# Optimization experiments

Measured on AMD Instinct MI355X. Metric: run time of the kernel, lower is better.

Reference implementation:

```python
import jax, jax.numpy as jnp
import numpy as np

B, C, W, H = 4, 64, 64, 64
CQK = C // 8  # query/key channels


def setup_inputs() -> dict:
    key = jax.random.key(0)
    ks = jax.random.split(key, 8)
    s = 0.05
    return {
        "x": jax.random.normal(ks[0], (B, C, W, H), jnp.float32),
        "Wq": jax.random.normal(ks[1], (CQK, C), jnp.float32) * s,
        "bq": jax.random.normal(ks[2], (CQK,), jnp.float32) * s,
        "Wk": jax.random.normal(ks[3], (CQK, C), jnp.float32) * s,
        "bk": jax.random.normal(ks[4], (CQK,), jnp.float32) * s,
        "Wv": jax.random.normal(ks[5], (C, C), jnp.float32) * s,
        "bv": jax.random.normal(ks[6], (C,), jnp.float32) * s,
        # torch init is zeros; use a nonzero value so the attention path is exercised
        "gamma": jax.random.normal(ks[7], (1,), jnp.float32) * s,
    }


def reference(x, Wq, bq, Wk, bk, Wv, bv, gamma):
    b, c, w, h = x.shape
    n = w * h
    xf = x.reshape(b, c, n)  # B, C, N
    # 1x1 convs == per-pixel linear maps
    q = jnp.einsum("oc,bcn->bno", Wq, xf) + bq           # B, N, Cqk
    k = jnp.einsum("oc,bcn->bon", Wk, xf) + bk[:, None]   # B, Cqk, N
    energy = jnp.einsum("bno,bom->bnm", q, k)             # B, N, N
    attn = jax.nn.softmax(energy, axis=-1)                # B, N, N
    v = jnp.einsum("oc,bcn->bon", Wv, xf) + bv[:, None]   # B, C, N
    # out[b,c,j] = sum_n v[b,c,n] * attn[j,n]  (bmm with attention^T)
    out = jnp.einsum("bcn,bjn->bcj", v, attn)
    out = out.reshape(b, c, w, h)
    return gamma * out + x
```

## Files before the change

### kernel.cpp

```cpp
#include <hip/hip_runtime.h>

typedef short s16x8 __attribute__((ext_vector_type(8)));
typedef float f32x4 __attribute__((ext_vector_type(4)));
typedef float f32x16 __attribute__((ext_vector_type(16)));
typedef unsigned u32x4 __attribute__((ext_vector_type(4)));

#define BB 4
#define NN 4096
#define LOG2E 1.4426950408889634f

__device__ __forceinline__ unsigned short f2bf(float f) {
    unsigned int u = __builtin_bit_cast(unsigned int, f);
    u += 0x7fff + ((u >> 16) & 1);
    return (unsigned short)(u >> 16);
}

__device__ __forceinline__ unsigned pk2(float lo, float hi) {
    return __builtin_amdgcn_perm(__builtin_bit_cast(unsigned, hi),
                                 __builtin_bit_cast(unsigned, lo), 0x07060302u);
}

__device__ __forceinline__ void pl32swap(unsigned &a, unsigned &b) {
    asm volatile("v_permlane32_swap_b32 %0, %1" : "+v"(a), "+v"(b));
}

__global__ __launch_bounds__(256) void proj_kernel(
    const float* __restrict__ x,
    const float* __restrict__ Wq, const float* __restrict__ bq,
    const float* __restrict__ Wk, const float* __restrict__ bk,
    const float* __restrict__ Wv, const float* __restrict__ bv,
    unsigned short* __restrict__ Qw, unsigned short* __restrict__ Kw,
    unsigned short* __restrict__ Vc)
{
    __shared__ __attribute__((aligned(16))) unsigned short sW[80 * 72];
    __shared__ __attribute__((aligned(16))) unsigned short xT[64 * 72];
    __shared__ float sb[80];

    int tid = threadIdx.x;
    int b  = blockIdx.x >> 6;
    int n0 = (blockIdx.x & 63) << 6;

    for (int i = tid; i < 1280; i += 256) {
        int o = i >> 4, c4 = (i & 15) << 2;
        const float* src = (o < 8) ? &Wq[o * 64 + c4]
                         : ((o < 16) ? &Wk[(o - 8) * 64 + c4]
                                     : &Wv[(o - 16) * 64 + c4]);
        float4 v = *(const float4*)src;
        float sc = (o < 8) ? LOG2E : 1.f;
        sW[o * 72 + c4 + 0] = f2bf(v.x * sc);
        sW[o * 72 + c4 + 1] = f2bf(v.y * sc);
        sW[o * 72 + c4 + 2] = f2bf(v.z * sc);
        sW[o * 72 + c4 + 3] = f2bf(v.w * sc);
    }
    if (tid < 80)
        sb[tid] = (tid < 8) ? bq[tid] * LOG2E
                            : ((tid < 16) ? bk[tid - 8] : bv[tid - 16]);
    for (int i = tid; i < 1024; i += 256) {
        int c = i >> 4, p4 = (i & 15) << 2;
        float4 v = *(const float4*)&x[(((size_t)b * 64 + c) << 12) + n0 + p4];
        xT[(p4 + 0) * 72 + c] = f2bf(v.x);
        xT[(p4 + 1) * 72 + c] = f2bf(v.y);
        xT[(p4 + 2) * 72 + c] = f2bf(v.z);
        xT[(p4 + 3) * 72 + c] = f2bf(v.w);
    }
    __syncthreads();

    int w = tid >> 6, l = tid & 63, g = l >> 4, q16 = l & 15;
    int pix = w * 16 + q16;

    s16x8 bf0 = *(const s16x8*)&xT[pix * 72 + g * 8];
    s16x8 bf1 = *(const s16x8*)&xT[pix * 72 + 32 + g * 8];

    s16x8 a0[5], a1[5];
#pragma unroll
    for (int ot = 0; ot < 5; ++ot) {
        a0[ot] = *(const s16x8*)&sW[(ot * 16 + q16) * 72 + g * 8];
        a1[ot] = *(const s16x8*)&sW[(ot * 16 + q16) * 72 + 32 + g * 8];
    }
    __syncthreads();

    unsigned short* sV = xT;
    size_t base16 = ((size_t)(b << 12) + n0 + pix) << 4;

#pragma unroll
    for (int ot = 0; ot < 5; ++ot) {
        f32x4 acc = {0.f, 0.f, 0.f, 0.f};
        acc = __builtin_amdgcn_mfma_f32_16x16x32_bf16(a0[ot], bf0, acc, 0, 0, 0);
        acc = __builtin_amdgcn_mfma_f32_16x16x32_bf16(a1[ot], bf1, acc, 0, 0, 0);
#pragma unroll
        for (int r = 0; r < 4; ++r) {
            int orow = ot * 16 + g * 4 + r;
            unsigned short hv = f2bf(acc[r] + sb[orow]);
            if (ot == 0) {
                if (orow < 8) {
                    Qw[base16 + orow] = hv;
                    Qw[base16 + orow + 8] = 0;
                } else {
                    Kw[base16 + orow - 8] = hv;
                    Kw[base16 + orow] = 0;
                }
            } else {
                sV[(orow - 16) * 72 + pix] = hv;
            }
        }
    }
    __syncthreads();

#pragma unroll
    for (int i = tid; i < 512; i += 256) {
        int jj = i >> 6, c = i & 63;
        u32x4 v = *(const u32x4*)&sV[c * 72 + jj * 8];
        int jglob = ((blockIdx.x & 63) << 3) + jj;
        *(u32x4*)&Vc[(((size_t)b * 512 + jglob) * 64 + c) * 8] = v;
    }
}

__global__ __launch_bounds__(512, 2) void attn_kernel(
    const unsigned short* __restrict__ Qw, const unsigned short* __restrict__ Kw,
    const unsigned short* __restrict__ Vc, const float* __restrict__ x,
    const float* __restrict__ gamma, float* __restrict__ outp)
{
    __shared__ __attribute__((aligned(16))) float sO[64 * 36];
    __shared__ float sL[8 * 32];
    __shared__ float sGL[32];

    int tid = threadIdx.x;
    int w = tid >> 6, l = tid & 63, r31 = l & 31, hi = l >> 5;
    int p = blockIdx.x;
    int xcd = p & 7, kgrp = p >> 3;
    int b = xcd >> 1;
    int n0 = (((kgrp << 1) | (xcd & 1))) << 5;
    float gm = gamma[0];

    s16x8 qf = *(const s16x8*)((const char*)Qw + ((size_t)b << 17)
                               + ((size_t)(n0 + r31) << 5) + (hi << 4));
    const char* KbW = (const char*)Kw + ((size_t)b << 17) + (w << 14)
                    + (r31 << 5) + (hi << 4);
    const char* VcB = (const char*)Vc + ((size_t)b << 19) + (w << 16)
                    + (hi << 10) + (r31 << 4);

    f32x16 zz;
#pragma unroll
    for (int i = 0; i < 16; ++i) zz[i] = 0.f;

    f32x16 acc0, acc1;
#pragma unroll
    for (int i = 0; i < 16; ++i) { acc0[i] = 0.f; acc1[i] = 0.f; }
    float la = 0.f;

    s16x8 K_a, A0_a, A1_a, B0_a, B1_a;
    s16x8 K_b, A0_b, A1_b, B0_b, B1_b;

#define LOADSET(S, kp, vp) do {                                             \
        K_##S  = *(const s16x8*)(kp);                                       \
        A0_##S = *(const s16x8*)(vp);                                       \
        B0_##S = *(const s16x8*)((vp) + 512);                               \
        A1_##S = *(const s16x8*)((vp) + 2048);                              \
        B1_##S = *(const s16x8*)((vp) + 2560);                              \
    } while (0)

#define STEP(S) do {                                                        \
        f32x16 E = __builtin_amdgcn_mfma_f32_32x32x16_bf16(K_##S, qf, zz, 0, 0, 0); \
        _Pragma("unroll")                                                   \
        for (int i = 0; i < 16; ++i) E[i] = __builtin_amdgcn_exp2f(E[i]);   \
        la += (((E[0] + E[1]) + (E[2] + E[3])) + ((E[4] + E[5]) + (E[6] + E[7]))) \
            + (((E[8] + E[9]) + (E[10] + E[11])) + ((E[12] + E[13]) + (E[14] + E[15]))); \
        unsigned x0 = pk2(E[0], E[1]),   x1 = pk2(E[2], E[3]);              \
        unsigned x2 = pk2(E[4], E[5]),   x3 = pk2(E[6], E[7]);              \
        unsigned x4 = pk2(E[8], E[9]),   x5 = pk2(E[10], E[11]);            \
        unsigned x6 = pk2(E[12], E[13]), x7 = pk2(E[14], E[15]);            \
        pl32swap(x0, x2); pl32swap(x1, x3);                                 \
        pl32swap(x4, x6); pl32swap(x5, x7);                                 \
        u32x4 u0 = {x0, x1, x2, x3}, u1 = {x4, x5, x6, x7};                 \
        s16x8 pf0 = __builtin_bit_cast(s16x8, u0);                          \
        s16x8 pf1 = __builtin_bit_cast(s16x8, u1);                          \
        acc0 = __builtin_amdgcn_mfma_f32_32x32x16_bf16(A0_##S, pf0, acc0, 0, 0, 0); \
        acc0 = __builtin_amdgcn_mfma_f32_32x32x16_bf16(A1_##S, pf1, acc0, 0, 0, 0); \
        acc1 = __builtin_amdgcn_mfma_f32_32x32x16_bf16(B0_##S, pf0, acc1, 0, 0, 0); \
        acc1 = __builtin_amdgcn_mfma_f32_32x32x16_bf16(B1_##S, pf1, acc1, 0, 0, 0); \
    } while (0)

    const char* ka = KbW;
    const char* va = VcB;
    const char* kb = KbW + 1024;
    const char* vb = VcB + 4096;

    LOADSET(a, ka, va);
    LOADSET(b, kb, vb);

#pragma unroll 1
    for (int tt = 0; tt < 7; ++tt) {
        ka += 2048; va += 8192;
        STEP(a);
        LOADSET(a, ka, va);
        kb += 2048; vb += 8192;
        STEP(b);
        LOADSET(b, kb, vb);
    }
    STEP(a);
    STEP(b);

#undef LOADSET
#undef STEP

    la += __shfl_xor(la, 32);
    if (l < 32) sL[w * 32 + l] = la;

#pragma unroll
    for (int s = 0; s < 8; ++s) {
        __syncthreads();
#pragma unroll
        for (int B = 0; B < 8; ++B) {
            if (((w + s) & 7) == B) {
                const int R2 = B & 3;
                float e0 = (B < 4) ? acc0[R2 * 4 + 0] : acc1[R2 * 4 + 0];
                float e1 = (B < 4) ? acc0[R2 * 4 + 1] : acc1[R2 * 4 + 1];
                float e2 = (B < 4) ? acc0[R2 * 4 + 2] : acc1[R2 * 4 + 2];
                float e3 = (B < 4) ? acc0[R2 * 4 + 3] : acc1[R2 * 4 + 3];
                float* pp = &sO[(B * 8 + hi * 4) * 36 + r31];
                if (s == 0) {
                    pp[0] = e0; pp[36] = e1; pp[72] = e2; pp[108] = e3;
                } else {
                    pp[0] += e0; pp[36] += e1; pp[72] += e2; pp[108] += e3;
                }
            }
        }
    }
    __syncthreads();

    if (tid < 32) {
        float L = 0.f;
#pragma unroll
        for (int wk2 = 0; wk2 < 8; ++wk2) L += sL[wk2 * 32 + tid];
        sGL[tid] = gm / L;
    }
    __syncthreads();

    {
        int c = tid >> 3, qc = tid & 7;
        float4 o4 = *(const float4*)&sO[c * 36 + qc * 4];
        float4 g4 = *(const float4*)&sGL[qc * 4];
        size_t idx = (((size_t)b * 64 + c) << 12) + n0 + qc * 4;
        float4 x4v = *(const float4*)&x[idx];
        o4.x = o4.x * g4.x + x4v.x;
        o4.y = o4.y * g4.y + x4v.y;
        o4.z = o4.z * g4.z + x4v.z;
        o4.w = o4.w * g4.w + x4v.w;
        *(float4*)&outp[idx] = o4;
    }
}

extern "C" void kernel_launch(void* const* d_in, const int* in_sizes, int n_in,
                              void* d_out, int out_size, void* d_ws, size_t ws_size,
                              hipStream_t stream) {
    const float* x     = (const float*)d_in[0];
    const float* Wq    = (const float*)d_in[1];
    const float* bq    = (const float*)d_in[2];
    const float* Wk    = (const float*)d_in[3];
    const float* bk    = (const float*)d_in[4];
    const float* Wv    = (const float*)d_in[5];
    const float* bv    = (const float*)d_in[6];
    const float* gamma = (const float*)d_in[7];
    float* out = (float*)d_out;

    unsigned short* Qw = (unsigned short*)d_ws;
    unsigned short* Kw = Qw + (size_t)BB * NN * 16;
    unsigned short* Vc = Kw + (size_t)BB * NN * 16;

    proj_kernel<<<256, 256, 0, stream>>>(x, Wq, bq, Wk, bk, Wv, bv, Qw, Kw, Vc);
    attn_kernel<<<512, 512, 0, stream>>>(Qw, Kw, Vc, x, gamma, out);
}
```

Baseline: 29.74 us.

## Process 64 query rows per block with 16 waves sharing a KV split

Each attention block now handles 64 query rows instead of 32. It uses 1024 threads arranged as 2 query groups by 8 KV-split waves, which halves the grid to 256 blocks. The two query groups read the same K/V ranges, so that traffic can hit in cache, and the per-block fixed costs of reduction and epilogue are amortised over twice the work. In exchange there are fewer blocks for 256 CUs, a heavier block with barrier syncs across 16 waves, and a possibly lower occupancy bound.

```diff
diff --git a/kernel.cpp b/kernel.cpp
--- a/kernel.cpp
+++ b/kernel.cpp
@@ -115,28 +115,29 @@
     }
 }
 
-__global__ __launch_bounds__(512, 2) void attn_kernel(
+__global__ __launch_bounds__(1024) void attn_kernel(
     const unsigned short* __restrict__ Qw, const unsigned short* __restrict__ Kw,
     const unsigned short* __restrict__ Vc, const float* __restrict__ x,
     const float* __restrict__ gamma, float* __restrict__ outp)
 {
-    __shared__ __attribute__((aligned(16))) float sO[64 * 36];
-    __shared__ float sL[8 * 32];
-    __shared__ float sGL[32];
+    __shared__ __attribute__((aligned(16))) float sO[64 * 68];
+    __shared__ float sL[8 * 64];
+    __shared__ float sGL[64];
 
     int tid = threadIdx.x;
     int w = tid >> 6, l = tid & 63, r31 = l & 31, hi = l >> 5;
+    int wq = w >> 3, wk = w & 7;
     int p = blockIdx.x;
-    int xcd = p & 7, kgrp = p >> 3;
+    int xcd = p & 7, qgrp = p >> 3;
     int b = xcd >> 1;
-    int n0 = (((kgrp << 1) | (xcd & 1))) << 5;
+    int n0 = ((qgrp << 1) | (xcd & 1)) << 6;
     float gm = gamma[0];
 
     s16x8 qf = *(const s16x8*)((const char*)Qw + ((size_t)b << 17)
-                               + ((size_t)(n0 + r31) << 5) + (hi << 4));
-    const char* KbW = (const char*)Kw + ((size_t)b << 17) + (w << 14)
+                               + ((size_t)(n0 + wq * 32 + r31) << 5) + (hi << 4));
+    const char* KbW = (const char*)Kw + ((size_t)b << 17) + (wk << 14)
                     + (r31 << 5) + (hi << 4);
-    const char* VcB = (const char*)Vc + ((size_t)b << 19) + (w << 16)
+    const char* VcB = (const char*)Vc + ((size_t)b << 19) + (wk << 16)
                     + (hi << 10) + (r31 << 4);
 
     f32x16 zz;
@@ -204,49 +205,43 @@
 #undef STEP
 
     la += __shfl_xor(la, 32);
-    if (l < 32) sL[w * 32 + l] = la;
+    if (l < 32) sL[wk * 64 + wq * 32 + l] = la;
 
 #pragma unroll
     for (int s = 0; s < 8; ++s) {
         __syncthreads();
 #pragma unroll
         for (int B = 0; B < 8; ++B) {
-            if (((w + s) & 7) == B) {
+            if (((wk + s) & 7) == B) {
                 const int R2 = B & 3;
                 float e0 = (B < 4) ? acc0[R2 * 4 + 0] : acc1[R2 * 4 + 0];
                 float e1 = (B < 4) ? acc0[R2 * 4 + 1] : acc1[R2 * 4 + 1];
                 float e2 = (B < 4) ? acc0[R2 * 4 + 2] : acc1[R2 * 4 + 2];
                 float e3 = (B < 4) ? acc0[R2 * 4 + 3] : acc1[R2 * 4 + 3];
-                float* pp = &sO[(B * 8 + hi * 4) * 36 + r31];
+                float* pp = &sO[(B * 8 + hi * 4) * 68 + wq * 32 + r31];
                 if (s == 0) {
-                    pp[0] = e0; pp[36] = e1; pp[72] = e2; pp[108] = e3;
+                    pp[0] = e0; pp[68] = e1; pp[136] = e2; pp[204] = e3;
                 } else {
-                    pp[0] += e0; pp[36] += e1; pp[72] += e2; pp[108] += e3;
+                    pp[0] += e0; pp[68] += e1; pp[136] += e2; pp[204] += e3;
                 }
             }
         }
     }
     __syncthreads();
 
-    if (tid < 32) {
+    if (tid < 64) {
         float L = 0.f;
 #pragma unroll
-        for (int wk2 = 0; wk2 < 8; ++wk2) L += sL[wk2 * 32 + tid];
+        for (int wk2 = 0; wk2 < 8; ++wk2) L += sL[wk2 * 64 + tid];
         sGL[tid] = gm / L;
     }
     __syncthreads();
 
-    {
-        int c = tid >> 3, qc = tid & 7;
-        float4 o4 = *(const float4*)&sO[c * 36 + qc * 4];
-        float4 g4 = *(const float4*)&sGL[qc * 4];
-        size_t idx = (((size_t)b * 64 + c) << 12) + n0 + qc * 4;
-        float4 x4v = *(const float4*)&x[idx];
-        o4.x = o4.x * g4.x + x4v.x;
-        o4.y = o4.y * g4.y + x4v.y;
-        o4.z = o4.z * g4.z + x4v.z;
-        o4.w = o4.w * g4.w + x4v.w;
-        *(float4*)&outp[idx] = o4;
+#pragma unroll
+    for (int pp = 0; pp < 4; ++pp) {
+        int c = pp * 16 + w;
+        size_t idx = (((size_t)b * 64 + c) << 12) + n0 + l;
+        outp[idx] = sGL[l] * sO[c * 68 + l] + x[idx];
     }
 }
 
@@ -268,5 +263,5 @@
     unsigned short* Vc = Kw + (size_t)BB * NN * 16;
 
     proj_kernel<<<256, 256, 0, stream>>>(x, Wq, bq, Wk, bk, Wv, bv, Qw, Kw, Vc);
-    attn_kernel<<<512, 512, 0, stream>>>(Qw, Kw, Vc, x, gamma, out);
-}
+    attn_kernel<<<256, 1024, 0, stream>>>(Qw, Kw, Vc, x, gamma, out);
+}
```

Result: no change. 29.76 us (+0.1%).
